# Kernel optimization log

Measured on AMD Instinct MI355X. Metric: run time of the kernel, lower is better.

## Reference

```python
import jax, jax.numpy as jnp
import numpy as np

B, T, D, ACT, H = 4096, 128, 64, 2, 64

def setup_inputs() -> dict:
    key = jax.random.key(0)
    ks = jax.random.split(key, 8)
    s = 1.0 / np.sqrt(H)
    return {
        "s0": jax.random.normal(ks[0], (B, D), jnp.float32),
        "a": jax.random.normal(ks[1], (B, T, ACT), jnp.float32),
        "w_ih": jax.random.uniform(ks[2], (3 * H, D + ACT), jnp.float32, -s, s),
        "w_hh": jax.random.uniform(ks[3], (3 * H, H), jnp.float32, -s, s),
        "b_ih": jax.random.uniform(ks[4], (3 * H,), jnp.float32, -s, s),
        "b_hh": jax.random.uniform(ks[5], (3 * H,), jnp.float32, -s, s),
        "w_out": jax.random.uniform(ks[6], (D, H), jnp.float32, -s, s),
        "b_out": jax.random.uniform(ks[7], (D,), jnp.float32, -s, s),
    }

def reference(s0, a, w_ih, w_hh, b_ih, b_hh, w_out, b_out):
    # PyTorch GRUCell convention: gates ordered (r, z, n)
    h0 = jnp.zeros((s0.shape[0], w_hh.shape[1]), s0.dtype)

    def step(carry, a_t):
        h, s = carry
        x = jnp.concatenate([s, a_t], axis=-1)              # [B, D+ACT]
        gi = x @ w_ih.T + b_ih                              # [B, 3H]
        gh = h @ w_hh.T + b_hh                              # [B, 3H]
        i_r, i_z, i_n = jnp.split(gi, 3, axis=-1)
        h_r, h_z, h_n = jnp.split(gh, 3, axis=-1)
        r = jax.nn.sigmoid(i_r + h_r)
        z = jax.nn.sigmoid(i_z + h_z)
        n = jnp.tanh(i_n + r * h_n)
        h_new = (1.0 - z) * n + z * h
        s_new = h_new @ w_out.T + b_out                     # [B, D]
        return (h_new, s_new), s_new

    a_tbd = jnp.swapaxes(a, 0, 1)                           # [T, B, ACT]
    _, outs = jax.lax.scan(step, (h0, s0), a_tbd)           # outs: [T, B, D]
    return jnp.swapaxes(outs, 0, 1)                         # [B, T, D]
```

## Files before the change

### kernel.cpp

```cpp
#include <hip/hip_runtime.h>
#include <hip/hip_bf16.h>

typedef __attribute__((ext_vector_type(8))) short bf16x8;
typedef __attribute__((ext_vector_type(4))) float f32x4;
typedef __attribute__((ext_vector_type(2))) float f32x2;

typedef bf16x8 bf16x8_a __attribute__((may_alias));
typedef f32x4  f32x4_a  __attribute__((may_alias));
typedef f32x2  f32x2_a  __attribute__((may_alias));
typedef unsigned short u16a __attribute__((may_alias));
typedef unsigned int u32;

__device__ __forceinline__ float fexp2(float x) {
  float r; asm("v_exp_f32 %0, %1" : "=v"(r) : "v"(x)); return r;
}
__device__ __forceinline__ float frcp(float x) {
  float r; asm("v_rcp_f32 %0, %1" : "=v"(r) : "v"(x)); return r;
}
__device__ __forceinline__ float sigf(float x) {
  return frcp(1.f + fexp2(x * -1.44269504f));
}
__device__ __forceinline__ float tanhf_(float x) {
  return 1.f - 2.f * frcp(1.f + fexp2(x * 2.88539008f));
}
__device__ __forceinline__ u32 cvtpk(float lo, float hi) {
  u32 r; asm("v_cvt_pk_bf16_f32 %0, %1, %2" : "=v"(r) : "v"(lo), "v"(hi)); return r;
}

#define LDS_WG   0
#define LDS_HB   24576
#define LDS_SIZE 28672

__device__ __forceinline__ void stbf(char* smem, int byteoff, float v) {
  union { __hip_bfloat16 b; unsigned short u; } cv;
  cv.b = __float2bfloat16(v);
  *(u16a*)(smem + byteoff) = cv.u;
}
__device__ __forceinline__ void st16(char* smem, int byteoff, unsigned short v) {
  *(u16a*)(smem + byteoff) = v;
}

__device__ __forceinline__ bf16x8 packf8(const float* v) {
  bf16x8 r;
  #pragma unroll
  for (int j = 0; j < 8; ++j) {
    union { __hip_bfloat16 b; short u; } cv;
    cv.b = __float2bfloat16(v[j]);
    r[j] = cv.u;
  }
  return r;
}

__device__ __forceinline__ void xbar() {
  asm volatile("s_waitcnt lgkmcnt(0)\n\ts_barrier" ::: "memory");
}

__global__ __launch_bounds__(256, 1)
void gru_fused(const float* __restrict__ s0, const float* __restrict__ a,
               const float* __restrict__ w_ih, const float* __restrict__ w_hh,
               const float* __restrict__ b_ih, const float* __restrict__ b_hh,
               const float* __restrict__ w_out, const float* __restrict__ b_out,
               float* __restrict__ out)
{
  __shared__ __align__(16) char smem[LDS_SIZE];
  const int tid = threadIdx.x;
  const int l = tid & 63;
  const int w = tid >> 6;
  const int c = l & 15;
  const int g = l >> 4;
  const int b0 = blockIdx.x * 16;
  const int swzc = (c & 7) << 4;

  for (int idx = tid; idx < 16 * 64; idx += 256) {
    int r = idx >> 6, k = idx & 63;
    stbf(smem, LDS_HB + r * 128 + ((k * 2) ^ ((r & 7) << 4)), s0[(b0 + r) * 64 + k]);
  }

  bf16x8 bwo[4][2];
  #pragma unroll
  for (int i = 0; i < 4; ++i) {
    #pragma unroll
    for (int ks = 0; ks < 2; ++ks) {
      float tv[8];
      #pragma unroll
      for (int j = 0; j < 8; ++j)
        tv[j] = w_out[(ks * 32 + g * 8 + j) * 64 + c + 16 * i];
      bwo[i][ks] = packf8(tv);
    }
  }
  #pragma unroll
  for (int rr = 0; rr < 3; ++rr) {
    int rt = w + 4 * rr;
    bf16x8 wsa[2];
    #pragma unroll
    for (int ks = 0; ks < 2; ++ks) {
      float tv[8];
      #pragma unroll
      for (int u = 0; u < 4; ++u) {
        f32x2 t2 = *(const f32x2_a*)(w_ih + (16 * rt + c) * 66 + ks * 32 + g * 8 + 2 * u);
        tv[2 * u] = t2.x; tv[2 * u + 1] = t2.y;
      }
      wsa[ks] = packf8(tv);
    }
    f32x4 acc[4];
    #pragma unroll
    for (int i = 0; i < 4; ++i) {
      #pragma unroll
      for (int j = 0; j < 4; ++j) {
        int n = 16 * rt + 4 * g + j;
        acc[i][j] = (n < 128) ? w_hh[n * 64 + c + 16 * i] : 0.f;
      }
    }
    #pragma unroll
    for (int i = 0; i < 4; ++i)
      #pragma unroll
      for (int ks = 0; ks < 2; ++ks)
        acc[i] = __builtin_amdgcn_mfma_f32_16x16x32_bf16(wsa[ks], bwo[i][ks], acc[i], 0, 0, 0);
    #pragma unroll
    for (int i = 0; i < 4; ++i)
      #pragma unroll
      for (int j = 0; j < 4; ++j) {
        int n = 16 * rt + 4 * g + j;
        stbf(smem, LDS_WG + n * 128 + (((c + 16 * i) * 2) ^ ((n & 7) << 4)), acc[i][j]);
      }
  }

  const int nr = 16 * w + c, nz = 64 + nr, ni = 128 + nr;
  float bs_r = 0.f, bs_z = 0.f, bs_i = 0.f;
  for (int d = 0; d < 64; ++d) {
    float bo = b_out[d];
    bs_r += w_ih[nr * 66 + d] * bo;
    bs_z += w_ih[nz * 66 + d] * bo;
    bs_i += w_ih[ni * 66 + d] * bo;
  }
  const float wa0_r = w_ih[nr * 66 + 64], wa1_r = w_ih[nr * 66 + 65];
  const float wa0_z = w_ih[nz * 66 + 64], wa1_z = w_ih[nz * 66 + 65];
  const float wa0_i = w_ih[ni * 66 + 64], wa1_i = w_ih[ni * 66 + 65];
  const float pb_r = b_ih[nr] + b_hh[nr];
  const float pb_z = b_ih[nz] + b_hh[nz];
  const float pb_i = b_ih[ni];
  const float bias_r = pb_r + bs_r;
  const float bias_z = pb_z + bs_z;
  const float bias_i = pb_i + bs_i;
  const float bias_hn = b_hh[ni];
  const float bias_o = b_out[nr];

  bf16x8 whn[2], wo[2], wsr[2], wsz[2], wsi[2];
  #pragma unroll
  for (int ks = 0; ks < 2; ++ks) {
    float tv[8];
    f32x4 t4;
    t4 = *(const f32x4_a*)(w_hh + ni * 64 + ks * 32 + g * 8);
    tv[0] = t4.x; tv[1] = t4.y; tv[2] = t4.z; tv[3] = t4.w;
    t4 = *(const f32x4_a*)(w_hh + ni * 64 + ks * 32 + g * 8 + 4);
    tv[4] = t4.x; tv[5] = t4.y; tv[6] = t4.z; tv[7] = t4.w;
    whn[ks] = packf8(tv);
    t4 = *(const f32x4_a*)(w_out + nr * 64 + ks * 32 + g * 8);
    tv[0] = t4.x; tv[1] = t4.y; tv[2] = t4.z; tv[3] = t4.w;
    t4 = *(const f32x4_a*)(w_out + nr * 64 + ks * 32 + g * 8 + 4);
    tv[4] = t4.x; tv[5] = t4.y; tv[6] = t4.z; tv[7] = t4.w;
    wo[ks] = packf8(tv);
    #pragma unroll
    for (int u = 0; u < 4; ++u) {
      f32x2 t2 = *(const f32x2_a*)(w_ih + nr * 66 + ks * 32 + g * 8 + 2 * u);
      tv[2 * u] = t2.x; tv[2 * u + 1] = t2.y;
    }
    wsr[ks] = packf8(tv);
    #pragma unroll
    for (int u = 0; u < 4; ++u) {
      f32x2 t2 = *(const f32x2_a*)(w_ih + nz * 66 + ks * 32 + g * 8 + 2 * u);
      tv[2 * u] = t2.x; tv[2 * u + 1] = t2.y;
    }
    wsz[ks] = packf8(tv);
    #pragma unroll
    for (int u = 0; u < 4; ++u) {
      f32x2 t2 = *(const f32x2_a*)(w_ih + ni * 66 + ks * 32 + g * 8 + 2 * u);
      tv[2 * u] = t2.x; tv[2 * u + 1] = t2.y;
    }
    wsi[ks] = packf8(tv);
  }

  int aoff[4], ooff[4];
  #pragma unroll
  for (int j = 0; j < 4; ++j) {
    int gr = b0 + 4 * g + j;
    aoff[j] = gr * 256;
    ooff[j] = gr * 8192 + nr;
  }

  __syncthreads();

  bf16x8 wgr[2], wgz[2], wgi[2];
  #pragma unroll
  for (int ks = 0; ks < 2; ++ks) {
    wgr[ks] = *(const bf16x8_a*)(smem + LDS_WG + nr * 128 + ((ks * 64 + g * 16) ^ swzc));
    wgz[ks] = *(const bf16x8_a*)(smem + LDS_WG + nz * 128 + ((ks * 64 + g * 16) ^ swzc));
    wgi[ks] = *(const bf16x8_a*)(smem + LDS_WG + ni * 128 + ((ks * 64 + g * 16) ^ swzc));
  }

  bf16x8 sa[2];
  #pragma unroll
  for (int ks = 0; ks < 2; ++ks)
    sa[ks] = *(const bf16x8_a*)(smem + LDS_HB + c * 128 + ((ks * 64 + g * 16) ^ swzc));
  f32x4 ar, az, ai;
  #pragma unroll
  for (int j = 0; j < 4; ++j) {
    f32x2 av = *(const f32x2_a*)(a + aoff[j]);
    ar[j] = pb_r + av.x * wa0_r + av.y * wa1_r;
    az[j] = pb_z + av.x * wa0_z + av.y * wa1_z;
    ai[j] = pb_i + av.x * wa0_i + av.y * wa1_i;
  }
  #pragma unroll
  for (int ks = 0; ks < 2; ++ks) {
    ar = __builtin_amdgcn_mfma_f32_16x16x32_bf16(sa[ks], wsr[ks], ar, 0, 0, 0);
    az = __builtin_amdgcn_mfma_f32_16x16x32_bf16(sa[ks], wsz[ks], az, 0, 0, 0);
    ai = __builtin_amdgcn_mfma_f32_16x16x32_bf16(sa[ks], wsi[ks], ai, 0, 0, 0);
  }
  float hreg[4];
  #pragma unroll
  for (int j = 0; j < 4; ++j) {
    float r = sigf(ar[j]);
    float z = sigf(az[j]);
    float nn = tanhf_(ai[j] + r * bias_hn);
    hreg[j] = nn - z * nn;
  }
  {
    u32 p01 = cvtpk(hreg[0], hreg[1]);
    u32 p23 = cvtpk(hreg[2], hreg[3]);
    int r0 = 4 * g;
    st16(smem, LDS_HB + 2048 + (r0    ) * 128 + ((2 * nr) ^ (((r0    ) & 7) << 4)), (unsigned short)(p01));
    st16(smem, LDS_HB + 2048 + (r0 + 1) * 128 + ((2 * nr) ^ (((r0 + 1) & 7) << 4)), (unsigned short)(p01 >> 16));
    st16(smem, LDS_HB + 2048 + (r0 + 2) * 128 + ((2 * nr) ^ (((r0 + 2) & 7) << 4)), (unsigned short)(p23));
    st16(smem, LDS_HB + 2048 + (r0 + 3) * 128 + ((2 * nr) ^ (((r0 + 3) & 7) << 4)), (unsigned short)(p23 >> 16));
  }
  f32x2 avnA[4], avnB[4];
  #pragma unroll
  for (int j = 0; j < 4; ++j) {
    avnA[j] = *(const f32x2_a*)(a + 2 + aoff[j]);
    avnB[j] = *(const f32x2_a*)(a + 4 + aoff[j]);
  }
  xbar();

#define HALF_STEP(RB, WB, AV, APN, OB)                                         \
  {                                                                            \
    const char* hb = smem + LDS_HB + (RB) + c * 128;                           \
    bf16x8 ha0 = *(const bf16x8_a*)(hb + ((g * 16) ^ swzc));                   \
    bf16x8 ha1 = *(const bf16x8_a*)(hb + ((64 + g * 16) ^ swzc));              \
    f32x4 arr, azz;                                                            \
    _Pragma("unroll")                                                          \
    for (int j = 0; j < 4; ++j) {                                              \
      arr[j] = bias_r + AV[j].x * wa0_r + AV[j].y * wa1_r;                     \
      azz[j] = bias_z + AV[j].x * wa0_z + AV[j].y * wa1_z;                     \
    }                                                                          \
    f32x4 aii, ahh;                                                            \
    _Pragma("unroll")                                                          \
    for (int j = 0; j < 4; ++j) {                                              \
      aii[j] = bias_i + AV[j].x * wa0_i + AV[j].y * wa1_i;                     \
      ahh[j] = bias_hn;                                                        \
    }                                                                          \
    _Pragma("unroll")                                                          \
    for (int j = 0; j < 4; ++j)                                                \
      AV[j] = *(const f32x2_a*)((APN) + aoff[j]);                              \
    arr = __builtin_amdgcn_mfma_f32_16x16x32_bf16(ha0, wgr[0], arr, 0, 0, 0);  \
    arr = __builtin_amdgcn_mfma_f32_16x16x32_bf16(ha1, wgr[1], arr, 0, 0, 0);  \
    azz = __builtin_amdgcn_mfma_f32_16x16x32_bf16(ha0, wgz[0], azz, 0, 0, 0);  \
    azz = __builtin_amdgcn_mfma_f32_16x16x32_bf16(ha1, wgz[1], azz, 0, 0, 0);  \
    float r_[4], z_[4];                                                        \
    _Pragma("unroll")                                                          \
    for (int j = 0; j < 4; ++j) { r_[j] = sigf(arr[j]); z_[j] = sigf(azz[j]); }\
    aii = __builtin_amdgcn_mfma_f32_16x16x32_bf16(ha0, wgi[0], aii, 0, 0, 0);  \
    aii = __builtin_amdgcn_mfma_f32_16x16x32_bf16(ha1, wgi[1], aii, 0, 0, 0);  \
    ahh = __builtin_amdgcn_mfma_f32_16x16x32_bf16(ha0, whn[0], ahh, 0, 0, 0);  \
    ahh = __builtin_amdgcn_mfma_f32_16x16x32_bf16(ha1, whn[1], ahh, 0, 0, 0);  \
    float hv[4];                                                               \
    _Pragma("unroll")                                                          \
    for (int j = 0; j < 4; ++j) {                                              \
      float nn = tanhf_(aii[j] + r_[j] * ahh[j]);                              \
      float h = nn + z_[j] * (hreg[j] - nn);                                   \
      hv[j] = h; hreg[j] = h;                                                  \
    }                                                                          \
    {                                                                          \
      u32 p01 = cvtpk(hv[0], hv[1]);                                           \
      u32 p23 = cvtpk(hv[2], hv[3]);                                           \
      int r0 = 4 * g;                                                          \
      char* hbn = smem + LDS_HB + (WB);                                        \
      st16(hbn, (r0    ) * 128 + ((2 * nr) ^ (((r0    ) & 7) << 4)), (unsigned short)(p01));       \
      st16(hbn, (r0 + 1) * 128 + ((2 * nr) ^ (((r0 + 1) & 7) << 4)), (unsigned short)(p01 >> 16)); \
      st16(hbn, (r0 + 2) * 128 + ((2 * nr) ^ (((r0 + 2) & 7) << 4)), (unsigned short)(p23));       \
      st16(hbn, (r0 + 3) * 128 + ((2 * nr) ^ (((r0 + 3) & 7) << 4)), (unsigned short)(p23 >> 16)); \
    }                                                                          \
    f32x4 ao = f32x4{bias_o, bias_o, bias_o, bias_o};                          \
    ao = __builtin_amdgcn_mfma_f32_16x16x32_bf16(ha0, wo[0], ao, 0, 0, 0);     \
    ao = __builtin_amdgcn_mfma_f32_16x16x32_bf16(ha1, wo[1], ao, 0, 0, 0);     \
    {                                                                          \
      float* ob = (OB);                                                        \
      _Pragma("unroll")                                                        \
      for (int j = 0; j < 4; ++j) ob[ooff[j]] = ao[j];                         \
    }                                                                          \
    xbar();                                                                    \
  }

  #pragma unroll 1
  for (int tp = 0; tp < 63; ++tp) {
    const int t1 = 2 * tp + 1;
    HALF_STEP(2048, 0, avnA, a + 2 * (t1 + 2), out + (size_t)(t1 - 1) * 64);
    const int t2n = (t1 + 3 <= 127) ? (t1 + 3) : 127;
    HALF_STEP(0, 2048, avnB, a + 2 * t2n, out + (size_t)t1 * 64);
  }

  HALF_STEP(2048, 0, avnA, a + 2 * 127, out + (size_t)126 * 64);

  {
    const char* hb = smem + LDS_HB + 0 + c * 128;
    bf16x8 ha0 = *(const bf16x8_a*)(hb + ((g * 16) ^ swzc));
    bf16x8 ha1 = *(const bf16x8_a*)(hb + ((64 + g * 16) ^ swzc));
    f32x4 ao = f32x4{bias_o, bias_o, bias_o, bias_o};
    ao = __builtin_amdgcn_mfma_f32_16x16x32_bf16(ha0, wo[0], ao, 0, 0, 0);
    ao = __builtin_amdgcn_mfma_f32_16x16x32_bf16(ha1, wo[1], ao, 0, 0, 0);
    float* ob = out + (size_t)127 * 64;
    #pragma unroll
    for (int j = 0; j < 4; ++j)
      ob[ooff[j]] = ao[j];
  }
#undef HALF_STEP
}

extern "C" void kernel_launch(void* const* d_in, const int* in_sizes, int n_in,
                              void* d_out, int out_size, void* d_ws, size_t ws_size,
                              hipStream_t stream) {
  const float* s0    = (const float*)d_in[0];
  const float* a     = (const float*)d_in[1];
  const float* w_ih  = (const float*)d_in[2];
  const float* w_hh  = (const float*)d_in[3];
  const float* b_ih  = (const float*)d_in[4];
  const float* b_hh  = (const float*)d_in[5];
  const float* w_out = (const float*)d_in[6];
  const float* b_out = (const float*)d_in[7];
  float* out = (float*)d_out;
  hipLaunchKernelGGL(gru_fused, dim3(4096 / 16), dim3(256), 0, stream,
                     s0, a, w_ih, w_hh, b_ih, b_hh, w_out, b_out, out);
}
```

Measured before the change: 75.16 us.

## Split GRU step across two wave groups with r gate exchanged via LDS

Doubles the block to 512 threads and specializes the waves. Waves 0-3 compute the r gate and the output projection. Waves 4-7 compute the z, input-n and hidden-n gates and update the hidden state, reading r from a new LDS slot after an extra barrier. This shortens the serial MFMA and transcendental chain each wave runs per timestep. In exchange it adds a second barrier per half-step and an LDS round trip for r.

```diff
diff --git a/kernel.cpp b/kernel.cpp
--- a/kernel.cpp
+++ b/kernel.cpp
@@ -8,6 +8,7 @@
 typedef bf16x8 bf16x8_a __attribute__((may_alias));
 typedef f32x4  f32x4_a  __attribute__((may_alias));
 typedef f32x2  f32x2_a  __attribute__((may_alias));
+typedef float  f32a     __attribute__((may_alias));
 typedef unsigned short u16a __attribute__((may_alias));
 typedef unsigned int u32;
 
@@ -29,7 +30,8 @@
 
 #define LDS_WG   0
 #define LDS_HB   24576
-#define LDS_SIZE 28672
+#define LDS_RZ   28672
+#define LDS_SIZE 32768
 
 __device__ __forceinline__ void stbf(char* smem, int byteoff, float v) {
   union { __hip_bfloat16 b; unsigned short u; } cv;
@@ -55,7 +57,7 @@
   asm volatile("s_waitcnt lgkmcnt(0)\n\ts_barrier" ::: "memory");
 }
 
-__global__ __launch_bounds__(256, 1)
+__global__ __launch_bounds__(512, 1)
 void gru_fused(const float* __restrict__ s0, const float* __restrict__ a,
                const float* __restrict__ w_ih, const float* __restrict__ w_hh,
                const float* __restrict__ b_ih, const float* __restrict__ b_hh,
@@ -66,12 +68,14 @@
   const int tid = threadIdx.x;
   const int l = tid & 63;
   const int w = tid >> 6;
+  const bool isA = (w < 4);
+  const int wa = w & 3;
   const int c = l & 15;
   const int g = l >> 4;
   const int b0 = blockIdx.x * 16;
   const int swzc = (c & 7) << 4;
 
-  for (int idx = tid; idx < 16 * 64; idx += 256) {
+  for (int idx = tid; idx < 16 * 64; idx += 512) {
     int r = idx >> 6, k = idx & 63;
     stbf(smem, LDS_HB + r * 128 + ((k * 2) ^ ((r & 7) << 4)), s0[(b0 + r) * 64 + k]);
   }
@@ -89,43 +93,45 @@
     }
   }
   #pragma unroll
-  for (int rr = 0; rr < 3; ++rr) {
-    int rt = w + 4 * rr;
-    bf16x8 wsa[2];
-    #pragma unroll
-    for (int ks = 0; ks < 2; ++ks) {
-      float tv[8];
-      #pragma unroll
-      for (int u = 0; u < 4; ++u) {
-        f32x2 t2 = *(const f32x2_a*)(w_ih + (16 * rt + c) * 66 + ks * 32 + g * 8 + 2 * u);
-        tv[2 * u] = t2.x; tv[2 * u + 1] = t2.y;
-      }
-      wsa[ks] = packf8(tv);
-    }
-    f32x4 acc[4];
-    #pragma unroll
-    for (int i = 0; i < 4; ++i) {
-      #pragma unroll
-      for (int j = 0; j < 4; ++j) {
-        int n = 16 * rt + 4 * g + j;
-        acc[i][j] = (n < 128) ? w_hh[n * 64 + c + 16 * i] : 0.f;
-      }
-    }
-    #pragma unroll
-    for (int i = 0; i < 4; ++i)
-      #pragma unroll
-      for (int ks = 0; ks < 2; ++ks)
-        acc[i] = __builtin_amdgcn_mfma_f32_16x16x32_bf16(wsa[ks], bwo[i][ks], acc[i], 0, 0, 0);
-    #pragma unroll
-    for (int i = 0; i < 4; ++i)
-      #pragma unroll
-      for (int j = 0; j < 4; ++j) {
-        int n = 16 * rt + 4 * g + j;
-        stbf(smem, LDS_WG + n * 128 + (((c + 16 * i) * 2) ^ ((n & 7) << 4)), acc[i][j]);
-      }
-  }
-
-  const int nr = 16 * w + c, nz = 64 + nr, ni = 128 + nr;
+  for (int rr = 0; rr < 2; ++rr) {
+    int rt = w + 8 * rr;
+    if (rt < 12) {
+      bf16x8 wsa[2];
+      #pragma unroll
+      for (int ks = 0; ks < 2; ++ks) {
+        float tv[8];
+        #pragma unroll
+        for (int u = 0; u < 4; ++u) {
+          f32x2 t2 = *(const f32x2_a*)(w_ih + (16 * rt + c) * 66 + ks * 32 + g * 8 + 2 * u);
+          tv[2 * u] = t2.x; tv[2 * u + 1] = t2.y;
+        }
+        wsa[ks] = packf8(tv);
+      }
+      f32x4 acc[4];
+      #pragma unroll
+      for (int i = 0; i < 4; ++i) {
+        #pragma unroll
+        for (int j = 0; j < 4; ++j) {
+          int n = 16 * rt + 4 * g + j;
+          acc[i][j] = (n < 128) ? w_hh[n * 64 + c + 16 * i] : 0.f;
+        }
+      }
+      #pragma unroll
+      for (int i = 0; i < 4; ++i)
+        #pragma unroll
+        for (int ks = 0; ks < 2; ++ks)
+          acc[i] = __builtin_amdgcn_mfma_f32_16x16x32_bf16(wsa[ks], bwo[i][ks], acc[i], 0, 0, 0);
+      #pragma unroll
+      for (int i = 0; i < 4; ++i)
+        #pragma unroll
+        for (int j = 0; j < 4; ++j) {
+          int n = 16 * rt + 4 * g + j;
+          stbf(smem, LDS_WG + n * 128 + (((c + 16 * i) * 2) ^ ((n & 7) << 4)), acc[i][j]);
+        }
+    }
+  }
+
+  const int nr = 16 * wa + c, nz = 64 + nr, ni = 128 + nr;
   float bs_r = 0.f, bs_z = 0.f, bs_i = 0.f;
   for (int d = 0; d < 64; ++d) {
     float bo = b_out[d];
@@ -145,39 +151,29 @@
   const float bias_hn = b_hh[ni];
   const float bias_o = b_out[nr];
 
-  bf16x8 whn[2], wo[2], wsr[2], wsz[2], wsi[2];
-  #pragma unroll
-  for (int ks = 0; ks < 2; ++ks) {
-    float tv[8];
-    f32x4 t4;
-    t4 = *(const f32x4_a*)(w_hh + ni * 64 + ks * 32 + g * 8);
-    tv[0] = t4.x; tv[1] = t4.y; tv[2] = t4.z; tv[3] = t4.w;
-    t4 = *(const f32x4_a*)(w_hh + ni * 64 + ks * 32 + g * 8 + 4);
-    tv[4] = t4.x; tv[5] = t4.y; tv[6] = t4.z; tv[7] = t4.w;
-    whn[ks] = packf8(tv);
-    t4 = *(const f32x4_a*)(w_out + nr * 64 + ks * 32 + g * 8);
-    tv[0] = t4.x; tv[1] = t4.y; tv[2] = t4.z; tv[3] = t4.w;
-    t4 = *(const f32x4_a*)(w_out + nr * 64 + ks * 32 + g * 8 + 4);
-    tv[4] = t4.x; tv[5] = t4.y; tv[6] = t4.z; tv[7] = t4.w;
-    wo[ks] = packf8(tv);
-    #pragma unroll
-    for (int u = 0; u < 4; ++u) {
-      f32x2 t2 = *(const f32x2_a*)(w_ih + nr * 66 + ks * 32 + g * 8 + 2 * u);
-      tv[2 * u] = t2.x; tv[2 * u + 1] = t2.y;
-    }
-    wsr[ks] = packf8(tv);
-    #pragma unroll
-    for (int u = 0; u < 4; ++u) {
-      f32x2 t2 = *(const f32x2_a*)(w_ih + nz * 66 + ks * 32 + g * 8 + 2 * u);
-      tv[2 * u] = t2.x; tv[2 * u + 1] = t2.y;
-    }
-    wsz[ks] = packf8(tv);
-    #pragma unroll
-    for (int u = 0; u < 4; ++u) {
-      f32x2 t2 = *(const f32x2_a*)(w_ih + ni * 66 + ks * 32 + g * 8 + 2 * u);
-      tv[2 * u] = t2.x; tv[2 * u + 1] = t2.y;
-    }
-    wsi[ks] = packf8(tv);
+  bf16x8 wo[2], whn[2];
+  if (isA) {
+    #pragma unroll
+    for (int ks = 0; ks < 2; ++ks) {
+      float tv[8];
+      f32x4 t4;
+      t4 = *(const f32x4_a*)(w_out + nr * 64 + ks * 32 + g * 8);
+      tv[0] = t4.x; tv[1] = t4.y; tv[2] = t4.z; tv[3] = t4.w;
+      t4 = *(const f32x4_a*)(w_out + nr * 64 + ks * 32 + g * 8 + 4);
+      tv[4] = t4.x; tv[5] = t4.y; tv[6] = t4.z; tv[7] = t4.w;
+      wo[ks] = packf8(tv);
+    }
+  } else {
+    #pragma unroll
+    for (int ks = 0; ks < 2; ++ks) {
+      float tv[8];
+      f32x4 t4;
+      t4 = *(const f32x4_a*)(w_hh + ni * 64 + ks * 32 + g * 8);
+      tv[0] = t4.x; tv[1] = t4.y; tv[2] = t4.z; tv[3] = t4.w;
+      t4 = *(const f32x4_a*)(w_hh + ni * 64 + ks * 32 + g * 8 + 4);
+      tv[4] = t4.x; tv[5] = t4.y; tv[6] = t4.z; tv[7] = t4.w;
+      whn[ks] = packf8(tv);
+    }
   }
 
   int aoff[4], ooff[4];
@@ -187,44 +183,73 @@
     aoff[j] = gr * 256;
     ooff[j] = gr * 8192 + nr;
   }
+  char* const rzbase = smem + LDS_RZ + wa * 256 + l * 4;
 
   __syncthreads();
 
   bf16x8 wgr[2], wgz[2], wgi[2];
-  #pragma unroll
-  for (int ks = 0; ks < 2; ++ks) {
-    wgr[ks] = *(const bf16x8_a*)(smem + LDS_WG + nr * 128 + ((ks * 64 + g * 16) ^ swzc));
-    wgz[ks] = *(const bf16x8_a*)(smem + LDS_WG + nz * 128 + ((ks * 64 + g * 16) ^ swzc));
-    wgi[ks] = *(const bf16x8_a*)(smem + LDS_WG + ni * 128 + ((ks * 64 + g * 16) ^ swzc));
-  }
-
-  bf16x8 sa[2];
-  #pragma unroll
-  for (int ks = 0; ks < 2; ++ks)
-    sa[ks] = *(const bf16x8_a*)(smem + LDS_HB + c * 128 + ((ks * 64 + g * 16) ^ swzc));
-  f32x4 ar, az, ai;
-  #pragma unroll
-  for (int j = 0; j < 4; ++j) {
-    f32x2 av = *(const f32x2_a*)(a + aoff[j]);
-    ar[j] = pb_r + av.x * wa0_r + av.y * wa1_r;
-    az[j] = pb_z + av.x * wa0_z + av.y * wa1_z;
-    ai[j] = pb_i + av.x * wa0_i + av.y * wa1_i;
-  }
-  #pragma unroll
-  for (int ks = 0; ks < 2; ++ks) {
-    ar = __builtin_amdgcn_mfma_f32_16x16x32_bf16(sa[ks], wsr[ks], ar, 0, 0, 0);
-    az = __builtin_amdgcn_mfma_f32_16x16x32_bf16(sa[ks], wsz[ks], az, 0, 0, 0);
-    ai = __builtin_amdgcn_mfma_f32_16x16x32_bf16(sa[ks], wsi[ks], ai, 0, 0, 0);
-  }
-  float hreg[4];
-  #pragma unroll
-  for (int j = 0; j < 4; ++j) {
-    float r = sigf(ar[j]);
-    float z = sigf(az[j]);
-    float nn = tanhf_(ai[j] + r * bias_hn);
-    hreg[j] = nn - z * nn;
-  }
-  {
+  if (isA) {
+    #pragma unroll
+    for (int ks = 0; ks < 2; ++ks)
+      wgr[ks] = *(const bf16x8_a*)(smem + LDS_WG + nr * 128 + ((ks * 64 + g * 16) ^ swzc));
+  } else {
+    #pragma unroll
+    for (int ks = 0; ks < 2; ++ks) {
+      wgz[ks] = *(const bf16x8_a*)(smem + LDS_WG + nz * 128 + ((ks * 64 + g * 16) ^ swzc));
+      wgi[ks] = *(const bf16x8_a*)(smem + LDS_WG + ni * 128 + ((ks * 64 + g * 16) ^ swzc));
+    }
+  }
+
+  float hreg[4] = {0.f, 0.f, 0.f, 0.f};
+  if (!isA) {
+    bf16x8 wsr[2], wsz[2], wsi[2];
+    #pragma unroll
+    for (int ks = 0; ks < 2; ++ks) {
+      float tv[8];
+      #pragma unroll
+      for (int u = 0; u < 4; ++u) {
+        f32x2 t2 = *(const f32x2_a*)(w_ih + nr * 66 + ks * 32 + g * 8 + 2 * u);
+        tv[2 * u] = t2.x; tv[2 * u + 1] = t2.y;
+      }
+      wsr[ks] = packf8(tv);
+      #pragma unroll
+      for (int u = 0; u < 4; ++u) {
+        f32x2 t2 = *(const f32x2_a*)(w_ih + nz * 66 + ks * 32 + g * 8 + 2 * u);
+        tv[2 * u] = t2.x; tv[2 * u + 1] = t2.y;
+      }
+      wsz[ks] = packf8(tv);
+      #pragma unroll
+      for (int u = 0; u < 4; ++u) {
+        f32x2 t2 = *(const f32x2_a*)(w_ih + ni * 66 + ks * 32 + g * 8 + 2 * u);
+        tv[2 * u] = t2.x; tv[2 * u + 1] = t2.y;
+      }
+      wsi[ks] = packf8(tv);
+    }
+    bf16x8 sa[2];
+    #pragma unroll
+    for (int ks = 0; ks < 2; ++ks)
+      sa[ks] = *(const bf16x8_a*)(smem + LDS_HB + c * 128 + ((ks * 64 + g * 16) ^ swzc));
+    f32x4 ar, az, ai;
+    #pragma unroll
+    for (int j = 0; j < 4; ++j) {
+      f32x2 av = *(const f32x2_a*)(a + aoff[j]);
+      ar[j] = pb_r + av.x * wa0_r + av.y * wa1_r;
+      az[j] = pb_z + av.x * wa0_z + av.y * wa1_z;
+      ai[j] = pb_i + av.x * wa0_i + av.y * wa1_i;
+    }
+    #pragma unroll
+    for (int ks = 0; ks < 2; ++ks) {
+      ar = __builtin_amdgcn_mfma_f32_16x16x32_bf16(sa[ks], wsr[ks], ar, 0, 0, 0);
+      az = __builtin_amdgcn_mfma_f32_16x16x32_bf16(sa[ks], wsz[ks], az, 0, 0, 0);
+      ai = __builtin_amdgcn_mfma_f32_16x16x32_bf16(sa[ks], wsi[ks], ai, 0, 0, 0);
+    }
+    #pragma unroll
+    for (int j = 0; j < 4; ++j) {
+      float r = sigf(ar[j]);
+      float z = sigf(az[j]);
+      float nn = tanhf_(ai[j] + r * bias_hn);
+      hreg[j] = nn - z * nn;
+    }
     u32 p01 = cvtpk(hreg[0], hreg[1]);
     u32 p23 = cvtpk(hreg[2], hreg[3]);
     int r0 = 4 * g;
@@ -246,40 +271,60 @@
     const char* hb = smem + LDS_HB + (RB) + c * 128;                           \
     bf16x8 ha0 = *(const bf16x8_a*)(hb + ((g * 16) ^ swzc));                   \
     bf16x8 ha1 = *(const bf16x8_a*)(hb + ((64 + g * 16) ^ swzc));              \
-    f32x4 arr, azz;                                                            \
-    _Pragma("unroll")                                                          \
-    for (int j = 0; j < 4; ++j) {                                              \
-      arr[j] = bias_r + AV[j].x * wa0_r + AV[j].y * wa1_r;                     \
-      azz[j] = bias_z + AV[j].x * wa0_z + AV[j].y * wa1_z;                     \
+    float z_[4];                                                               \
+    f32x4 aii, ahh, ao;                                                        \
+    if (isA) {                                                                 \
+      f32x4 arr;                                                               \
+      _Pragma("unroll")                                                        \
+      for (int j = 0; j < 4; ++j) {                                            \
+        arr[j] = bias_r + AV[j].x * wa0_r + AV[j].y * wa1_r;                   \
+        ao[j] = bias_o;                                                        \
+      }                                                                        \
+      _Pragma("unroll")                                                        \
+      for (int j = 0; j < 4; ++j) AV[j] = *(const f32x2_a*)((APN) + aoff[j]);  \
+      arr = __builtin_amdgcn_mfma_f32_16x16x32_bf16(ha0, wgr[0], arr, 0, 0, 0);\
+      arr = __builtin_amdgcn_mfma_f32_16x16x32_bf16(ha1, wgr[1], arr, 0, 0, 0);\
+      ao  = __builtin_amdgcn_mfma_f32_16x16x32_bf16(ha0, wo[0],  ao,  0, 0, 0);\
+      ao  = __builtin_amdgcn_mfma_f32_16x16x32_bf16(ha1, wo[1],  ao,  0, 0, 0);\
+      _Pragma("unroll")                                                        \
+      for (int j = 0; j < 4; ++j)                                              \
+        *(f32a*)(rzbase + j * 1024) = sigf(arr[j]);                            \
+    } else {                                                                   \
+      f32x4 azz;                                                               \
+      _Pragma("unroll")                                                        \
+      for (int j = 0; j < 4; ++j) {                                            \
+        azz[j] = bias_z + AV[j].x * wa0_z + AV[j].y * wa1_z;                   \
+        aii[j] = bias_i + AV[j].x * wa0_i + AV[j].y * wa1_i;                   \
+        ahh[j] = bias_hn;                                                      \
+      }                                                                        \
+      _Pragma("unroll")                                                        \
+      for (int j = 0; j < 4; ++j) AV[j] = *(const f32x2_a*)((APN) + aoff[j]);  \
+      azz = __builtin_amdgcn_mfma_f32_16x16x32_bf16(ha0, wgz[0], azz, 0, 0, 0);\
+      azz = __builtin_amdgcn_mfma_f32_16x16x32_bf16(ha1, wgz[1], azz, 0, 0, 0);\
+      aii = __builtin_amdgcn_mfma_f32_16x16x32_bf16(ha0, wgi[0], aii, 0, 0, 0);\
+      aii = __builtin_amdgcn_mfma_f32_16x16x32_bf16(ha1, wgi[1], aii, 0, 0, 0);\
+      ahh = __builtin_amdgcn_mfma_f32_16x16x32_bf16(ha0, whn[0], ahh, 0, 0, 0);\
+      ahh = __builtin_amdgcn_mfma_f32_16x16x32_bf16(ha1, whn[1], ahh, 0, 0, 0);\
+      _Pragma("unroll")                                                        \
+      for (int j = 0; j < 4; ++j) z_[j] = sigf(azz[j]);                        \
     }                                                                          \
-    f32x4 aii, ahh;                                                            \
-    _Pragma("unroll")                                                          \
-    for (int j = 0; j < 4; ++j) {                                              \
-      aii[j] = bias_i + AV[j].x * wa0_i + AV[j].y * wa1_i;                     \
-      ahh[j] = bias_hn;                                                        \
-    }                                                                          \
-    _Pragma("unroll")                                                          \
-    for (int j = 0; j < 4; ++j)                                                \
-      AV[j] = *(const f32x2_a*)((APN) + aoff[j]);                              \
-    arr = __builtin_amdgcn_mfma_f32_16x16x32_bf16(ha0, wgr[0], arr, 0, 0, 0);  \
-    arr = __builtin_amdgcn_mfma_f32_16x16x32_bf16(ha1, wgr[1], arr, 0, 0, 0);  \
-    azz = __builtin_amdgcn_mfma_f32_16x16x32_bf16(ha0, wgz[0], azz, 0, 0, 0);  \
-    azz = __builtin_amdgcn_mfma_f32_16x16x32_bf16(ha1, wgz[1], azz, 0, 0, 0);  \
-    float r_[4], z_[4];                                                        \
-    _Pragma("unroll")                                                          \
-    for (int j = 0; j < 4; ++j) { r_[j] = sigf(arr[j]); z_[j] = sigf(azz[j]); }\
-    aii = __builtin_amdgcn_mfma_f32_16x16x32_bf16(ha0, wgi[0], aii, 0, 0, 0);  \
-    aii = __builtin_amdgcn_mfma_f32_16x16x32_bf16(ha1, wgi[1], aii, 0, 0, 0);  \
-    ahh = __builtin_amdgcn_mfma_f32_16x16x32_bf16(ha0, whn[0], ahh, 0, 0, 0);  \
-    ahh = __builtin_amdgcn_mfma_f32_16x16x32_bf16(ha1, whn[1], ahh, 0, 0, 0);  \
-    float hv[4];                                                               \
-    _Pragma("unroll")                                                          \
-    for (int j = 0; j < 4; ++j) {                                              \
-      float nn = tanhf_(aii[j] + r_[j] * ahh[j]);                              \
-      float h = nn + z_[j] * (hreg[j] - nn);                                   \
-      hv[j] = h; hreg[j] = h;                                                  \
-    }                                                                          \
-    {                                                                          \
+    xbar();                                           \
+    if (isA) {                                                                 \
+      float* ob = (OB);                                                        \
+      _Pragma("unroll")                                                        \
+      for (int j = 0; j < 4; ++j) ob[ooff[j]] = ao[j];                         \
+    } else {                                                                   \
+      float r_[4];                                                             \
+      _Pragma("unroll")                                                        \
+      for (int j = 0; j < 4; ++j)                                              \
+        r_[j] = *(const f32a*)(rzbase + j * 1024);                             \
+      float hv[4];                                                             \
+      _Pragma("unroll")                                                        \
+      for (int j = 0; j < 4; ++j) {                                            \
+        float nn = tanhf_(aii[j] + r_[j] * ahh[j]);                            \
+        float h = nn + z_[j] * (hreg[j] - nn);                                 \
+        hv[j] = h; hreg[j] = h;                                                \
+      }                                                                        \
       u32 p01 = cvtpk(hv[0], hv[1]);                                           \
       u32 p23 = cvtpk(hv[2], hv[3]);                                           \
       int r0 = 4 * g;                                                          \
@@ -289,15 +334,7 @@
       st16(hbn, (r0 + 2) * 128 + ((2 * nr) ^ (((r0 + 2) & 7) << 4)), (unsigned short)(p23));       \
       st16(hbn, (r0 + 3) * 128 + ((2 * nr) ^ (((r0 + 3) & 7) << 4)), (unsigned short)(p23 >> 16)); \
     }                                                                          \
-    f32x4 ao = f32x4{bias_o, bias_o, bias_o, bias_o};                          \
-    ao = __builtin_amdgcn_mfma_f32_16x16x32_bf16(ha0, wo[0], ao, 0, 0, 0);     \
-    ao = __builtin_amdgcn_mfma_f32_16x16x32_bf16(ha1, wo[1], ao, 0, 0, 0);     \
-    {                                                                          \
-      float* ob = (OB);                                                        \
-      _Pragma("unroll")                                                        \
-      for (int j = 0; j < 4; ++j) ob[ooff[j]] = ao[j];                         \
-    }                                                                          \
-    xbar();                                                                    \
+    xbar();                                           \
   }
 
   #pragma unroll 1
@@ -310,7 +347,7 @@
 
   HALF_STEP(2048, 0, avnA, a + 2 * 127, out + (size_t)126 * 64);
 
-  {
+  if (isA) {
     const char* hb = smem + LDS_HB + 0 + c * 128;
     bf16x8 ha0 = *(const bf16x8_a*)(hb + ((g * 16) ^ swzc));
     bf16x8 ha1 = *(const bf16x8_a*)(hb + ((64 + g * 16) ^ swzc));
@@ -337,6 +374,6 @@
   const float* w_out = (const float*)d_in[6];
   const float* b_out = (const float*)d_in[7];
   float* out = (float*)d_out;
-  hipLaunchKernelGGL(gru_fused, dim3(4096 / 16), dim3(256), 0, stream,
+  hipLaunchKernelGGL(gru_fused, dim3(4096 / 16), dim3(512), 0, stream,
                      s0, a, w_ih, w_hh, b_ih, b_hh, w_out, b_out, out);
 }
```

Measured after the change: 94.82 us. 1.26x slower.

## Pack two 16-row batch tiles per 512-thread block and hoist output MFMA

Applied to the files above, without the earlier changes.

Each workgroup now processes 32 batch rows with 8 waves in two independent 4-wave groups. Each group has its own double-buffered hidden-state region in LDS. The grid halves, and a CU now holds two waves per SIMD, so one wave's latency in the serial recurrence can be hidden by the other. The output-projection MFMA is also issued right after the gate MFMAs and before the sigmoid work, to overlap the matrix and vector pipes. The risk is that only half as many CUs are occupied on the 256-CU part, and every barrier now has to synchronise 8 waves.

```diff
diff --git a/kernel.cpp b/kernel.cpp
--- a/kernel.cpp
+++ b/kernel.cpp
@@ -29,7 +29,7 @@
 
 #define LDS_WG   0
 #define LDS_HB   24576
-#define LDS_SIZE 28672
+#define LDS_SIZE 32768
 
 __device__ __forceinline__ void stbf(char* smem, int byteoff, float v) {
   union { __hip_bfloat16 b; unsigned short u; } cv;
@@ -55,7 +55,7 @@
   asm volatile("s_waitcnt lgkmcnt(0)\n\ts_barrier" ::: "memory");
 }
 
-__global__ __launch_bounds__(256, 1)
+__global__ __launch_bounds__(512, 1)
 void gru_fused(const float* __restrict__ s0, const float* __restrict__ a,
                const float* __restrict__ w_ih, const float* __restrict__ w_hh,
                const float* __restrict__ b_ih, const float* __restrict__ b_hh,
@@ -66,14 +66,18 @@
   const int tid = threadIdx.x;
   const int l = tid & 63;
   const int w = tid >> 6;
+  const int p = w >> 2;
+  const int wa = w & 3;
   const int c = l & 15;
   const int g = l >> 4;
-  const int b0 = blockIdx.x * 16;
+  const int b0 = blockIdx.x * 32;
   const int swzc = (c & 7) << 4;
-
-  for (int idx = tid; idx < 16 * 64; idx += 256) {
+  char* const hb_p = smem + LDS_HB + p * 2048;
+
+  for (int idx = tid; idx < 32 * 64; idx += 512) {
     int r = idx >> 6, k = idx & 63;
-    stbf(smem, LDS_HB + r * 128 + ((k * 2) ^ ((r & 7) << 4)), s0[(b0 + r) * 64 + k]);
+    stbf(smem, LDS_HB + (r >> 4) * 2048 + (r & 15) * 128 + ((k * 2) ^ ((r & 7) << 4)),
+         s0[(b0 + r) * 64 + k]);
   }
 
   bf16x8 bwo[4][2];
@@ -89,43 +93,45 @@
     }
   }
   #pragma unroll
-  for (int rr = 0; rr < 3; ++rr) {
-    int rt = w + 4 * rr;
-    bf16x8 wsa[2];
-    #pragma unroll
-    for (int ks = 0; ks < 2; ++ks) {
-      float tv[8];
-      #pragma unroll
-      for (int u = 0; u < 4; ++u) {
-        f32x2 t2 = *(const f32x2_a*)(w_ih + (16 * rt + c) * 66 + ks * 32 + g * 8 + 2 * u);
-        tv[2 * u] = t2.x; tv[2 * u + 1] = t2.y;
+  for (int rr = 0; rr < 2; ++rr) {
+    int rt = w + 8 * rr;
+    if (rt < 12) {
+      bf16x8 wsa[2];
+      #pragma unroll
+      for (int ks = 0; ks < 2; ++ks) {
+        float tv[8];
+        #pragma unroll
+        for (int u = 0; u < 4; ++u) {
+          f32x2 t2 = *(const f32x2_a*)(w_ih + (16 * rt + c) * 66 + ks * 32 + g * 8 + 2 * u);
+          tv[2 * u] = t2.x; tv[2 * u + 1] = t2.y;
+        }
+        wsa[ks] = packf8(tv);
       }
-      wsa[ks] = packf8(tv);
-    }
-    f32x4 acc[4];
-    #pragma unroll
-    for (int i = 0; i < 4; ++i) {
-      #pragma unroll
-      for (int j = 0; j < 4; ++j) {
-        int n = 16 * rt + 4 * g + j;
-        acc[i][j] = (n < 128) ? w_hh[n * 64 + c + 16 * i] : 0.f;
+      f32x4 acc[4];
+      #pragma unroll
+      for (int i = 0; i < 4; ++i) {
+        #pragma unroll
+        for (int j = 0; j < 4; ++j) {
+          int n = 16 * rt + 4 * g + j;
+          acc[i][j] = (n < 128) ? w_hh[n * 64 + c + 16 * i] : 0.f;
+        }
       }
-    }
-    #pragma unroll
-    for (int i = 0; i < 4; ++i)
-      #pragma unroll
-      for (int ks = 0; ks < 2; ++ks)
-        acc[i] = __builtin_amdgcn_mfma_f32_16x16x32_bf16(wsa[ks], bwo[i][ks], acc[i], 0, 0, 0);
-    #pragma unroll
-    for (int i = 0; i < 4; ++i)
-      #pragma unroll
-      for (int j = 0; j < 4; ++j) {
-        int n = 16 * rt + 4 * g + j;
-        stbf(smem, LDS_WG + n * 128 + (((c + 16 * i) * 2) ^ ((n & 7) << 4)), acc[i][j]);
-      }
-  }
-
-  const int nr = 16 * w + c, nz = 64 + nr, ni = 128 + nr;
+      #pragma unroll
+      for (int i = 0; i < 4; ++i)
+        #pragma unroll
+        for (int ks = 0; ks < 2; ++ks)
+          acc[i] = __builtin_amdgcn_mfma_f32_16x16x32_bf16(wsa[ks], bwo[i][ks], acc[i], 0, 0, 0);
+      #pragma unroll
+      for (int i = 0; i < 4; ++i)
+        #pragma unroll
+        for (int j = 0; j < 4; ++j) {
+          int n = 16 * rt + 4 * g + j;
+          stbf(smem, LDS_WG + n * 128 + (((c + 16 * i) * 2) ^ ((n & 7) << 4)), acc[i][j]);
+        }
+    }
+  }
+
+  const int nr = 16 * wa + c, nz = 64 + nr, ni = 128 + nr;
   float bs_r = 0.f, bs_z = 0.f, bs_i = 0.f;
   for (int d = 0; d < 64; ++d) {
     float bo = b_out[d];
@@ -183,7 +189,7 @@
   int aoff[4], ooff[4];
   #pragma unroll
   for (int j = 0; j < 4; ++j) {
-    int gr = b0 + 4 * g + j;
+    int gr = b0 + 16 * p + 4 * g + j;
     aoff[j] = gr * 256;
     ooff[j] = gr * 8192 + nr;
   }
@@ -201,7 +207,7 @@
   bf16x8 sa[2];
   #pragma unroll
   for (int ks = 0; ks < 2; ++ks)
-    sa[ks] = *(const bf16x8_a*)(smem + LDS_HB + c * 128 + ((ks * 64 + g * 16) ^ swzc));
+    sa[ks] = *(const bf16x8_a*)(hb_p + c * 128 + ((ks * 64 + g * 16) ^ swzc));
   f32x4 ar, az, ai;
   #pragma unroll
   for (int j = 0; j < 4; ++j) {
@@ -228,10 +234,10 @@
     u32 p01 = cvtpk(hreg[0], hreg[1]);
     u32 p23 = cvtpk(hreg[2], hreg[3]);
     int r0 = 4 * g;
-    st16(smem, LDS_HB + 2048 + (r0    ) * 128 + ((2 * nr) ^ (((r0    ) & 7) << 4)), (unsigned short)(p01));
-    st16(smem, LDS_HB + 2048 + (r0 + 1) * 128 + ((2 * nr) ^ (((r0 + 1) & 7) << 4)), (unsigned short)(p01 >> 16));
-    st16(smem, LDS_HB + 2048 + (r0 + 2) * 128 + ((2 * nr) ^ (((r0 + 2) & 7) << 4)), (unsigned short)(p23));
-    st16(smem, LDS_HB + 2048 + (r0 + 3) * 128 + ((2 * nr) ^ (((r0 + 3) & 7) << 4)), (unsigned short)(p23 >> 16));
+    st16(hb_p, 4096 + (r0    ) * 128 + ((2 * nr) ^ (((r0    ) & 7) << 4)), (unsigned short)(p01));
+    st16(hb_p, 4096 + (r0 + 1) * 128 + ((2 * nr) ^ (((r0 + 1) & 7) << 4)), (unsigned short)(p01 >> 16));
+    st16(hb_p, 4096 + (r0 + 2) * 128 + ((2 * nr) ^ (((r0 + 2) & 7) << 4)), (unsigned short)(p23));
+    st16(hb_p, 4096 + (r0 + 3) * 128 + ((2 * nr) ^ (((r0 + 3) & 7) << 4)), (unsigned short)(p23 >> 16));
   }
   f32x2 avnA[4], avnB[4];
   #pragma unroll
@@ -243,20 +249,17 @@
 
 #define HALF_STEP(RB, WB, AV, APN, OB)                                         \
   {                                                                            \
-    const char* hb = smem + LDS_HB + (RB) + c * 128;                           \
+    const char* hb = hb_p + (RB) + c * 128;                                    \
     bf16x8 ha0 = *(const bf16x8_a*)(hb + ((g * 16) ^ swzc));                   \
     bf16x8 ha1 = *(const bf16x8_a*)(hb + ((64 + g * 16) ^ swzc));              \
-    f32x4 arr, azz;                                                            \
+    f32x4 arr, azz, aii, ahh, ao;                                              \
     _Pragma("unroll")                                                          \
     for (int j = 0; j < 4; ++j) {                                              \
       arr[j] = bias_r + AV[j].x * wa0_r + AV[j].y * wa1_r;                     \
       azz[j] = bias_z + AV[j].x * wa0_z + AV[j].y * wa1_z;                     \
-    }                                                                          \
-    f32x4 aii, ahh;                                                            \
-    _Pragma("unroll")                                                          \
-    for (int j = 0; j < 4; ++j) {                                              \
       aii[j] = bias_i + AV[j].x * wa0_i + AV[j].y * wa1_i;                     \
       ahh[j] = bias_hn;                                                        \
+      ao[j]  = bias_o;                                                         \
     }                                                                          \
     _Pragma("unroll")                                                          \
     for (int j = 0; j < 4; ++j)                                                \
@@ -265,13 +268,15 @@
     arr = __builtin_amdgcn_mfma_f32_16x16x32_bf16(ha1, wgr[1], arr, 0, 0, 0);  \
     azz = __builtin_amdgcn_mfma_f32_16x16x32_bf16(ha0, wgz[0], azz, 0, 0, 0);  \
     azz = __builtin_amdgcn_mfma_f32_16x16x32_bf16(ha1, wgz[1], azz, 0, 0, 0);  \
-    float r_[4], z_[4];                                                        \
-    _Pragma("unroll")                                                          \
-    for (int j = 0; j < 4; ++j) { r_[j] = sigf(arr[j]); z_[j] = sigf(azz[j]); }\
     aii = __builtin_amdgcn_mfma_f32_16x16x32_bf16(ha0, wgi[0], aii, 0, 0, 0);  \
     aii = __builtin_amdgcn_mfma_f32_16x16x32_bf16(ha1, wgi[1], aii, 0, 0, 0);  \
     ahh = __builtin_amdgcn_mfma_f32_16x16x32_bf16(ha0, whn[0], ahh, 0, 0, 0);  \
     ahh = __builtin_amdgcn_mfma_f32_16x16x32_bf16(ha1, whn[1], ahh, 0, 0, 0);  \
+    ao  = __builtin_amdgcn_mfma_f32_16x16x32_bf16(ha0, wo[0],  ao,  0, 0, 0);  \
+    ao  = __builtin_amdgcn_mfma_f32_16x16x32_bf16(ha1, wo[1],  ao,  0, 0, 0);  \
+    float r_[4], z_[4];                                                        \
+    _Pragma("unroll")                                                          \
+    for (int j = 0; j < 4; ++j) { r_[j] = sigf(arr[j]); z_[j] = sigf(azz[j]); }\
     float hv[4];                                                               \
     _Pragma("unroll")                                                          \
     for (int j = 0; j < 4; ++j) {                                              \
@@ -283,15 +288,12 @@
       u32 p01 = cvtpk(hv[0], hv[1]);                                           \
       u32 p23 = cvtpk(hv[2], hv[3]);                                           \
       int r0 = 4 * g;                                                          \
-      char* hbn = smem + LDS_HB + (WB);                                        \
+      char* hbn = hb_p + (WB);                                                 \
       st16(hbn, (r0    ) * 128 + ((2 * nr) ^ (((r0    ) & 7) << 4)), (unsigned short)(p01));       \
       st16(hbn, (r0 + 1) * 128 + ((2 * nr) ^ (((r0 + 1) & 7) << 4)), (unsigned short)(p01 >> 16)); \
       st16(hbn, (r0 + 2) * 128 + ((2 * nr) ^ (((r0 + 2) & 7) << 4)), (unsigned short)(p23));       \
       st16(hbn, (r0 + 3) * 128 + ((2 * nr) ^ (((r0 + 3) & 7) << 4)), (unsigned short)(p23 >> 16)); \
     }                                                                          \
-    f32x4 ao = f32x4{bias_o, bias_o, bias_o, bias_o};                          \
-    ao = __builtin_amdgcn_mfma_f32_16x16x32_bf16(ha0, wo[0], ao, 0, 0, 0);     \
-    ao = __builtin_amdgcn_mfma_f32_16x16x32_bf16(ha1, wo[1], ao, 0, 0, 0);     \
     {                                                                          \
       float* ob = (OB);                                                        \
       _Pragma("unroll")                                                        \
@@ -303,15 +305,15 @@
   #pragma unroll 1
   for (int tp = 0; tp < 63; ++tp) {
     const int t1 = 2 * tp + 1;
-    HALF_STEP(2048, 0, avnA, a + 2 * (t1 + 2), out + (size_t)(t1 - 1) * 64);
+    HALF_STEP(4096, 0, avnA, a + 2 * (t1 + 2), out + (size_t)(t1 - 1) * 64);
     const int t2n = (t1 + 3 <= 127) ? (t1 + 3) : 127;
-    HALF_STEP(0, 2048, avnB, a + 2 * t2n, out + (size_t)t1 * 64);
-  }
-
-  HALF_STEP(2048, 0, avnA, a + 2 * 127, out + (size_t)126 * 64);
+    HALF_STEP(0, 4096, avnB, a + 2 * t2n, out + (size_t)t1 * 64);
+  }
+
+  HALF_STEP(4096, 0, avnA, a + 2 * 127, out + (size_t)126 * 64);
 
   {
-    const char* hb = smem + LDS_HB + 0 + c * 128;
+    const char* hb = hb_p + 0 + c * 128;
     bf16x8 ha0 = *(const bf16x8_a*)(hb + ((g * 16) ^ swzc));
     bf16x8 ha1 = *(const bf16x8_a*)(hb + ((64 + g * 16) ^ swzc));
     f32x4 ao = f32x4{bias_o, bias_o, bias_o, bias_o};
@@ -337,6 +339,6 @@
   const float* w_out = (const float*)d_in[6];
   const float* b_out = (const float*)d_in[7];
   float* out = (float*)d_out;
-  hipLaunchKernelGGL(gru_fused, dim3(4096 / 16), dim3(256), 0, stream,
+  hipLaunchKernelGGL(gru_fused, dim3(4096 / 32), dim3(512), 0, stream,
                      s0, a, w_ih, w_hh, b_ih, b_hh, w_out, b_out, out);
 }
```

Measured after the change: 106.5 us. +41.7%, slower.
